# Kernel optimization log

Hardware: AMD Instinct MI355X
Metric: run time of the kernel (lower is better)

Reference implementation:

```python
import jax, jax.numpy as jnp
import numpy as np

D_STATE = 16
D_CONV = 4

def layernorm(x, g, b, eps=1e-5):
    m = jnp.mean(x, -1, keepdims=True)
    v = jnp.var(x, -1, keepdims=True)
    return (x - m) / jnp.sqrt(v + eps) * g + b

def conv1x1(x, w):  # x [b,h,w,cin], w [cin,cout]
    return jnp.einsum('bhwc,cd->bhwd', x, w)

def dwconv3x3(x, w):  # x [b,h,w,C], w [3,3,1,C] (HWIO, groups=C)
    return jax.lax.conv_general_dilated(x, w, (1, 1), 'SAME',
        dimension_numbers=('NHWC', 'HWIO', 'NHWC'),
        feature_group_count=x.shape[-1])

def causal_dwconv1d(x, w, b):  # x [B,L,D], w [K,1,D]; causal depthwise conv (Mamba d_conv=4)
    xp = jnp.pad(x, ((0, 0), (D_CONV - 1, 0), (0, 0)))
    y = jax.lax.conv_general_dilated(xp, w, (1,), 'VALID',
        dimension_numbers=('NWC', 'WIO', 'NWC'),
        feature_group_count=x.shape[-1])
    return y + b

def selective_scan(deltaA, deltaBx, C):
    # deltaA, deltaBx: [B,L,D,S]; C: [B,L,S] -> y: [B,L,D]
    def step(h, inp):
        dA, dBx, c = inp
        h = dA * h + dBx
        return h, jnp.einsum('bds,bs->bd', h, c)
    h0 = jnp.zeros(deltaA.shape[:1] + deltaA.shape[2:], deltaA.dtype)
    _, ys = jax.lax.scan(step, h0,
        (jnp.swapaxes(deltaA, 0, 1), jnp.swapaxes(deltaBx, 0, 1), jnp.swapaxes(C, 0, 1)))
    return jnp.swapaxes(ys, 0, 1)

def spa_ssm(x, in_w, conv_w, conv_b, xproj_w, dt_w, dt_b, Alog, D, out_w):
    # Mamba (slow path) applied to flattened spatial sequence; x: [b,h,w,c]
    b, h, w, c = x.shape
    L = h * w
    xs = x.reshape(b, L, c)
    di = Alog.shape[0]
    xz = xs @ in_w                       # [b,L,2*di]
    xi, z = xz[..., :di], xz[..., di:]
    xi = jax.nn.silu(causal_dwconv1d(xi, conv_w, conv_b))
    dbc = xi @ xproj_w                   # [b,L,dt_rank+2*S]
    dtr = dt_w.shape[0]
    dt = jax.nn.softplus(dbc[..., :dtr] @ dt_w + dt_b)   # [b,L,di]
    B = dbc[..., dtr:dtr + D_STATE]
    C = dbc[..., dtr + D_STATE:]
    A = -jnp.exp(Alog)                   # [di,S]
    deltaA = jnp.exp(dt[..., None] * A)                  # [b,L,di,S]
    deltaBx = (dt * xi)[..., None] * B[:, :, None, :]    # [b,L,di,S]
    y = selective_scan(deltaA, deltaBx, C) + D * xi
    y = y * jax.nn.silu(z)
    return (y @ out_w).reshape(b, h, w, c)

def camba_forward(x, ln1_g, ln1_b, vin_w1, vin_dw, vin_w2, vout_dw1, vout_dw2,
                  ssm_in_w, ssm_conv_w, ssm_conv_b, ssm_xproj_w, ssm_dt_w, ssm_dt_b,
                  ssm_Alog, ssm_D, ssm_out_w, ln2_g, ln2_b, ff_w1, ff_dw, ff_w2):
    x = jnp.transpose(x, (0, 2, 3, 1))   # [b,h,w,c]
    # ESSM: v_in_head = LN -> 1x1 -> dw3x3 -> GELU -> 1x1
    x0 = conv1x1(layernorm(x, ln1_g, ln1_b), vin_w1)
    x0 = jax.nn.gelu(dwconv3x3(x0, vin_dw), approximate=False)
    x0 = conv1x1(x0, vin_w2)
    y = spa_ssm(x0, ssm_in_w, ssm_conv_w, ssm_conv_b, ssm_xproj_w,
                ssm_dt_w, ssm_dt_b, ssm_Alog, ssm_D, ssm_out_w) + x0
    # v_out_head = dw3x3 -> GELU -> dw3x3, residual
    y = dwconv3x3(jax.nn.gelu(dwconv3x3(y, vout_dw1), approximate=False), vout_dw2) + y
    x = y + x                            # block residual
    # PreNorm FeedForward (mult=4): 1x1 -> LReLU -> dw3x3 -> LReLU -> 1x1
    t = layernorm(x, ln2_g, ln2_b)
    t = jax.nn.leaky_relu(conv1x1(t, ff_w1), 0.2)
    t = jax.nn.leaky_relu(dwconv3x3(t, ff_dw), 0.2)
    t = conv1x1(t, ff_w2)
    x = t + x
    return jnp.transpose(x, (0, 3, 1, 2))

def setup_inputs() -> dict:
    key = jax.random.key(0)
    ks = jax.random.split(key, 16)
    b, c, h, w = 8, 64, 64, 64
    di, ds, dtr = 128, 16, 4
    s = 0.05
    n = lambda k, shp: jax.random.normal(k, shp, jnp.float32) * s
    dt0 = jnp.exp(jax.random.uniform(ks[1], (di,)) * (np.log(0.1) - np.log(1e-3)) + np.log(1e-3))
    return dict(
        x=jax.random.normal(ks[0], (b, c, h, w), jnp.float32),
        ln1_g=jnp.ones(c), ln1_b=jnp.zeros(c),
        vin_w1=n(ks[2], (c, c)), vin_dw=n(ks[3], (3, 3, 1, c)), vin_w2=n(ks[4], (c, c)),
        vout_dw1=n(ks[5], (3, 3, 1, c)), vout_dw2=n(ks[6], (3, 3, 1, c)),
        ssm_in_w=n(ks[7], (c, 2 * di)),
        ssm_conv_w=n(ks[8], (D_CONV, 1, di)), ssm_conv_b=jnp.zeros(di),
        ssm_xproj_w=n(ks[9], (di, dtr + 2 * ds)),
        ssm_dt_w=n(ks[10], (dtr, di)), ssm_dt_b=jnp.log(jnp.expm1(dt0)),
        ssm_Alog=jnp.log(jnp.broadcast_to(jnp.arange(1., ds + 1), (di, ds))),
        ssm_D=jnp.ones(di),
        ssm_out_w=n(ks[11], (di, c)),
        ln2_g=jnp.ones(c), ln2_b=jnp.zeros(c),
        ff_w1=n(ks[12], (c, 4 * c)), ff_dw=n(ks[13], (3, 3, 1, 4 * c)), ff_w2=n(ks[14], (4 * c, c)),
    )

def reference(x, ln1_g, ln1_b, vin_w1, vin_dw, vin_w2, vout_dw1, vout_dw2,
              ssm_in_w, ssm_conv_w, ssm_conv_b, ssm_xproj_w, ssm_dt_w, ssm_dt_b,
              ssm_Alog, ssm_D, ssm_out_w, ln2_g, ln2_b, ff_w1, ff_dw, ff_w2):
    return camba_forward(x, ln1_g, ln1_b, vin_w1, vin_dw, vin_w2, vout_dw1, vout_dw2,
                         ssm_in_w, ssm_conv_w, ssm_conv_b, ssm_xproj_w, ssm_dt_w, ssm_dt_b,
                         ssm_Alog, ssm_D, ssm_out_w, ln2_g, ln2_b, ff_w1, ff_dw, ff_w2)
```

## Files before the change

kernel.cpp:

```cpp
#include <hip/hip_runtime.h>
#include <hip/hip_bf16.h>
#include <math.h>

typedef unsigned short u16;
typedef __attribute__((ext_vector_type(8))) short s8v;
typedef __attribute__((ext_vector_type(4))) float f4v;

#define B_    8
#define C_    64
#define HW_   4096
#define NPIX  32768
#define DI    128
#define NCH   256
#define CHL   16

__device__ __forceinline__ float b2f(u16 v){ return __uint_as_float(((unsigned)v)<<16); }
__device__ __forceinline__ u16 f2b(float x){
  unsigned u = __float_as_uint(x);
  u += 0x7fff + ((u >> 16) & 1);
  return (u16)(u >> 16);
}
__device__ __forceinline__ float gelu_exact(float x){ return 0.5f*x*(1.0f+erff(x*0.70710678118654752f)); }
__device__ __forceinline__ float leaky02(float x){ return x>0.f ? x : 0.2f*x; }
__device__ __forceinline__ float softplus_(float x){ return fmaxf(x,0.f)+log1pf(__expf(-fabsf(x))); }
__device__ __forceinline__ float silu_(float x){ return x / (1.0f + __expf(-x)); }
__device__ __forceinline__ void unpack16(uint4 q0, uint4 q1, float* v){
  unsigned w[8]={q0.x,q0.y,q0.z,q0.w,q1.x,q1.y,q1.z,q1.w};
  #pragma unroll
  for(int j=0;j<8;j++){
    v[2*j]   = __uint_as_float(w[j]<<16);
    v[2*j+1] = __uint_as_float(w[j]&0xffff0000u);
  }
}

__global__ void k_prep(const float* __restrict__ vin_w1, const float* __restrict__ vin_w2,
                       const float* __restrict__ ssm_in_w, const float* __restrict__ xproj,
                       const float* __restrict__ dtw, const float* __restrict__ ssm_outw,
                       const float* __restrict__ ff_w1, const float* __restrict__ ff_w2,
                       u16* __restrict__ wv1, u16* __restrict__ wv2, u16* __restrict__ wsi,
                       u16* __restrict__ wdb, u16* __restrict__ wout, u16* __restrict__ wf1,
                       u16* __restrict__ wf2t){
  int g = blockIdx.x*256 + threadIdx.x;
  if(g < 4096){
    int n=g>>6, c=g&63;
    wv1[n*64+c]=f2b(vin_w1[c*64+n]);
    wv2[n*64+c]=f2b(vin_w2[c*64+n]);
  }
  if(g < 16384){
    int n=g>>6, c=g&63;
    wsi[n*64+c]=f2b(ssm_in_w[c*256+n]);
    wf1[n*64+c]=f2b(ff_w1[c*256+n]);
    int n2=g/256, k2=g%256;
    wf2t[n2*256+k2]=f2b(ff_w2[k2*64+n2]);
  }
  if(g < 8192){
    int n=g>>7, k=g&127;
    wout[n*128+k]=f2b(ssm_outw[k*64+n]);
  }
  if(g < 20480){
    int n=g/128, k=g%128;
    float v;
    if(n < 128){
      v = 0.f;
      for(int r=0;r<4;r++) v += xproj[k*36+r]*dtw[r*128+n];
    }else{
      v = xproj[k*36+4+(n-128)];
    }
    wdb[n*128+k]=f2b(v);
  }
}

__global__ __launch_bounds__(256) void k_trans_ln_mm(const float* __restrict__ x,
                     const float* __restrict__ g, const float* __restrict__ bta,
                     const u16* __restrict__ wT,
                     u16* __restrict__ xT, u16* __restrict__ outp){
  const int LDA = 72, NS = 4;
  __shared__ float tile[64][65];
  __shared__ __align__(16) u16 sA[64*LDA];
  __shared__ __align__(16) u16 sW[64*LDA];
  int tid = threadIdx.x;
  int blk = blockIdx.x;
  int b = blk >> 6;
  int hwb = (blk & 63) << 6;
  int lane = tid & 63, row = tid >> 6;
  const float* src = x + (size_t)b*C_*HW_;
  #pragma unroll
  for(int k=0;k<16;k++){
    int c = row + 4*k;
    tile[c][lane] = src[c*HW_ + hwb + lane];
  }
  for(int idx=tid; idx<64*8; idx+=256){
    int n = idx>>3, c8 = (idx&7)*8;
    *(uint4*)(sW + n*LDA + c8) = *(const uint4*)(wT + n*64 + c8);
  }
  __syncthreads();
  u16* dstT = xT + (size_t)b*HW_*C_;
  #pragma unroll
  for(int k=0;k<16;k++){
    int hwl = row + 4*k;
    dstT[(hwb+hwl)*C_ + lane] = f2b(tile[lane][hwl]);
  }
  float gg = g[lane], bb = bta[lane];
  #pragma unroll
  for(int i=0;i<16;i++){
    int hwl = row*16 + i;
    float v = tile[lane][hwl];
    float s = v, sq = v*v;
    #pragma unroll
    for(int o=32;o>0;o>>=1){ s += __shfl_xor(s,o); sq += __shfl_xor(sq,o); }
    float m = s*(1.f/64.f);
    float var = sq*(1.f/64.f) - m*m;
    float r = rsqrtf(var + 1e-5f);
    sA[hwl*LDA + lane] = f2b((v-m)*r*gg + bb);
  }
  __syncthreads();
  int ln = tid & 63, wv = tid >> 6;
  int mrow = ln & 15, quad = ln >> 4;
  f4v acc[NS];
  #pragma unroll
  for(int i=0;i<NS;i++) acc[i] = (f4v){0.f,0.f,0.f,0.f};
  const u16* aBase = sA + (wv*16 + mrow)*LDA + quad*8;
  const u16* wBase = sW + mrow*LDA + quad*8;
  #pragma unroll
  for(int kk=0; kk<64; kk+=32){
    s8v af = *(const s8v*)(aBase + kk);
    #pragma unroll
    for(int ns=0; ns<NS; ns++){
      s8v bf = *(const s8v*)(wBase + ns*16*LDA + kk);
      acc[ns] = __builtin_amdgcn_mfma_f32_16x16x32_bf16(af, bf, acc[ns], 0, 0, 0);
    }
  }
  int p0 = blk*64;
  int pr = p0 + wv*16 + quad*4;
  #pragma unroll
  for(int ns=0; ns<NS; ns++){
    int n = ns*16 + mrow;
    #pragma unroll
    for(int r=0;r<4;r++)
      outp[(size_t)(pr+r)*64 + n] = f2b(acc[ns][r]);
  }
}

__global__ __launch_bounds__(256) void k_dw3mm(const u16* __restrict__ in,
                     const float* __restrict__ dwgt, const u16* __restrict__ wT,
                     u16* __restrict__ x0){
  const int LDT = 72;
  __shared__ __align__(16) u16 sIn[10*10*64];
  __shared__ __align__(16) u16 sT[64*LDT];
  __shared__ __align__(16) u16 sW[64*LDT];
  int tid = threadIdx.x;
  int blk = blockIdx.x;
  int b = blk >> 6;
  int t6 = blk & 63;
  int h0 = (t6 >> 3) * 8, w0 = (t6 & 7) * 8;
  for(int idx=tid; idx<64*8; idx+=256){
    int n = idx>>3, c8 = (idx&7)*8;
    *(uint4*)(sW + n*LDT + c8) = *(const uint4*)(wT + n*64 + c8);
  }
  for(int q=tid; q<10*10*16; q+=256){
    int pp = q >> 4, c4 = q & 15;
    int hh = pp / 10, ww = pp % 10;
    int gh = h0-1+hh, gw = w0-1+ww;
    ushort4 v = make_ushort4(0,0,0,0);
    if((unsigned)gh < 64u && (unsigned)gw < 64u)
      v = *(const ushort4*)(in + (size_t)((b*64+gh)*64+gw)*64 + c4*4);
    *(ushort4*)(sIn + pp*64 + c4*4) = v;
  }
  __syncthreads();
  int c4 = tid & 15;
  #pragma unroll
  for(int pass=0; pass<4; pass++){
    int opix = pass*16 + (tid>>4);
    int oh = opix >> 3, ow = opix & 7;
    float a0=0.f,a1=0.f,a2=0.f,a3=0.f;
    #pragma unroll
    for(int kh=0;kh<3;kh++){
      #pragma unroll
      for(int kw=0;kw<3;kw++){
        ushort4 v = *(const ushort4*)(sIn + ((oh+kh)*10 + (ow+kw))*64 + c4*4);
        float4 wv = *(const float4*)(dwgt + (kh*3+kw)*64 + c4*4);
        a0 += b2f(v.x)*wv.x; a1 += b2f(v.y)*wv.y;
        a2 += b2f(v.z)*wv.z; a3 += b2f(v.w)*wv.w;
      }
    }
    ushort4 o; o.x=f2b(gelu_exact(a0)); o.y=f2b(gelu_exact(a1));
    o.z=f2b(gelu_exact(a2)); o.w=f2b(gelu_exact(a3));
    *(ushort4*)(sT + opix*LDT + c4*4) = o;
  }
  __syncthreads();
  int ln = tid & 63, wv = tid >> 6;
  int mrow = ln & 15, quad = ln >> 4;
  f4v acc[4];
  #pragma unroll
  for(int i=0;i<4;i++) acc[i] = (f4v){0.f,0.f,0.f,0.f};
  const u16* aBase = sT + (wv*16 + mrow)*LDT + quad*8;
  const u16* wBase = sW + mrow*LDT + quad*8;
  #pragma unroll
  for(int kk=0; kk<64; kk+=32){
    s8v af = *(const s8v*)(aBase + kk);
    #pragma unroll
    for(int ns=0; ns<4; ns++){
      s8v bf = *(const s8v*)(wBase + ns*16*LDT + kk);
      acc[ns] = __builtin_amdgcn_mfma_f32_16x16x32_bf16(af, bf, acc[ns], 0, 0, 0);
    }
  }
  #pragma unroll
  for(int ns=0; ns<4; ns++){
    int n = ns*16 + mrow;
    #pragma unroll
    for(int r=0;r<4;r++){
      int opix = wv*16 + quad*4 + r;
      int oh = opix >> 3, ow = opix & 7;
      size_t p = ((size_t)(b*64 + h0+oh)*64 + (w0+ow));
      x0[p*64 + n] = f2b(acc[ns][r]);
    }
  }
}

__global__ __launch_bounds__(256) void k_ssm_dtbc(const u16* __restrict__ wT,
                     const u16* __restrict__ x0,
                     const float* __restrict__ cw, const float* __restrict__ cb,
                     const u16* __restrict__ wdb, const float* __restrict__ dtbias,
                     const float* __restrict__ alog,
                     u16* __restrict__ xi, u16* __restrict__ zs,
                     u16* __restrict__ dtout, u16* __restrict__ bcout,
                     u16* __restrict__ Pb, u16* __restrict__ Qb){
  const int LDA=72, NS=16, LDY=136, LDWD=136, NS2=10, LDD=136;
  __shared__ __align__(16) u16 S[31616];
  u16* sW   = S;
  u16* sA   = S + 18432;
  u16* ubuf = S + 23040;
  u16* xiT  = S;
  u16* wdbS = S + 8704;
  u16* sdt  = S + 8704;
  u16* sbc2 = S + 17408;
  int tid = threadIdx.x;
  int p0 = blockIdx.x*64;
  int ln = tid & 63, wv = tid >> 6;
  int mrow = ln & 15, quad = ln >> 4;
  for(int idx=tid; idx<256*8; idx+=256){
    int n = idx>>3, c8 = (idx&7)*8;
    *(uint4*)(sW + n*LDA + c8) = *(const uint4*)(wT + n*64 + c8);
  }
  for(int g=tid; g<64*8; g+=256){
    int row = g >> 3, c8 = (g & 7)*8;
    *(uint4*)(sA + row*LDA + c8) = *(const uint4*)(x0 + (size_t)(p0+row)*64 + c8);
  }
  __syncthreads();
  f4v acc[NS];
  #pragma unroll
  for(int i=0;i<NS;i++) acc[i] = (f4v){0.f,0.f,0.f,0.f};
  const u16* aBase = sA + (wv*16 + mrow)*LDA + quad*8;
  const u16* wBase = sW + mrow*LDA + quad*8;
  #pragma unroll
  for(int kk=0; kk<64; kk+=32){
    s8v af = *(const s8v*)(aBase + kk);
    #pragma unroll
    for(int ns=0; ns<NS; ns++){
      s8v bf = *(const s8v*)(wBase + ns*16*LDA + kk);
      acc[ns] = __builtin_amdgcn_mfma_f32_16x16x32_bf16(af, bf, acc[ns], 0, 0, 0);
    }
  }
  bool bstart = ((p0 & 4095) == 0);
  for(int idx=tid; idx<384; idx+=256){
    int j = idx >> 7, n = idx & 127;
    float a2 = 0.f;
    if(!bstart){
      const u16* xr = x0 + (size_t)(p0-3+j)*64;
      #pragma unroll 8
      for(int c=0;c<64;c++) a2 += b2f(xr[c]) * b2f(sW[n*LDA+c]);
    }
    ubuf[j*128 + n] = f2b(a2);
  }
  int prl = wv*16 + quad*4;
  #pragma unroll
  for(int ns=0; ns<NS; ns++){
    int n = ns*16 + mrow;
    if(n < 128){
      #pragma unroll
      for(int r=0;r<4;r++) ubuf[(prl+r+3)*128 + n] = f2b(acc[ns][r]);
    }else{
      #pragma unroll
      for(int r=0;r<4;r++) zs[(size_t)(p0+prl+r)*128 + (n-128)] = f2b(silu_(acc[ns][r]));
    }
  }
  __syncthreads();
  int d4 = tid & 31;
  float4 cbv = *(const float4*)(cb + d4*4);
  for(int row = tid >> 5; row < 64; row += 8){
    float a0=cbv.x, a1=cbv.y, a2=cbv.z, a3=cbv.w;
    #pragma unroll
    for(int k=0;k<4;k++){
      ushort4 v = *(const ushort4*)(ubuf + (row+k)*128 + d4*4);
      float4 wv4 = *(const float4*)(cw + k*128 + d4*4);
      a0 += b2f(v.x)*wv4.x; a1 += b2f(v.y)*wv4.y;
      a2 += b2f(v.z)*wv4.z; a3 += b2f(v.w)*wv4.w;
    }
    ushort4 o; o.x=f2b(silu_(a0)); o.y=f2b(silu_(a1)); o.z=f2b(silu_(a2)); o.w=f2b(silu_(a3));
    *(ushort4*)(xi + (size_t)(p0+row)*128 + d4*4) = o;
    *(ushort4*)(xiT + row*LDY + d4*4) = o;
  }
  __syncthreads();
  for(int idx=tid; idx<160*16; idx+=256){
    int n = idx>>4, c8 = (idx&15)*8;
    *(uint4*)(wdbS + n*LDWD + c8) = *(const uint4*)(wdb + n*128 + c8);
  }
  __syncthreads();
  f4v acc2[NS2];
  #pragma unroll
  for(int i=0;i<NS2;i++) acc2[i] = (f4v){0.f,0.f,0.f,0.f};
  #pragma unroll
  for(int kk=0; kk<128; kk+=32){
    s8v af = *(const s8v*)(xiT + (wv*16+mrow)*LDY + kk + quad*8);
    #pragma unroll
    for(int ns=0; ns<NS2; ns++){
      s8v bf = *(const s8v*)(wdbS + (ns*16+mrow)*LDWD + kk + quad*8);
      acc2[ns] = __builtin_amdgcn_mfma_f32_16x16x32_bf16(af, bf, acc2[ns], 0, 0, 0);
    }
  }
  __syncthreads();
  int pr = p0 + prl;
  #pragma unroll
  for(int ns=0; ns<NS2; ns++){
    int n = ns*16 + mrow;
    if(n < 128){
      float bs = dtbias[n];
      #pragma unroll
      for(int r=0;r<4;r++){
        u16 dv = f2b(softplus_(acc2[ns][r] + bs));
        dtout[(size_t)(pr+r)*128 + n] = dv;
        sdt[(prl+r)*LDD + n] = dv;
      }
    }else{
      #pragma unroll
      for(int r=0;r<4;r++){
        u16 bv = f2b(acc2[ns][r]);
        bcout[(size_t)(pr+r)*32 + (n-128)] = bv;
        sbc2[(prl+r)*36 + (n-128)] = bv;
      }
    }
  }
  __syncthreads();
  {
    int d = tid & 127;
    int cp = tid >> 7;
    float A[16];
    #pragma unroll
    for(int s=0;s<16;s++) A[s] = -__expf(alog[d*16+s]);
    int bI = p0 >> 12;
    int chbase = (p0 & 4095) >> 4;
    for(int cc = 2*cp; cc < 2*cp+2; cc++){
      int r0 = cc*16;
      float Q[16], sumdt = 0.f;
      #pragma unroll
      for(int s=0;s<16;s++) Q[s] = 0.f;
      #pragma unroll
      for(int i=0;i<CHL;i++){
        float dtv = b2f(sdt[(r0+i)*LDD + d]);
        float uv  = dtv * b2f(xiT[(r0+i)*LDY + d]);
        sumdt += dtv;
        #pragma unroll
        for(int s=0;s<16;s++){
          float Bv = b2f(sbc2[(r0+i)*36 + s]);
          float a = __expf(dtv*A[s]);
          Q[s] = a*Q[s] + uv*Bv;
        }
      }
      int gidx = (chbase+cc)*16384 + (bI*128+d)*16;
      unsigned pw[8], qw[8];
      #pragma unroll
      for(int j=0;j<8;j++){
        pw[j] = (unsigned)f2b(__expf(A[2*j]*sumdt)) | ((unsigned)f2b(__expf(A[2*j+1]*sumdt))<<16);
        qw[j] = (unsigned)f2b(Q[2*j]) | ((unsigned)f2b(Q[2*j+1])<<16);
      }
      *(uint4*)(Pb+gidx)   = make_uint4(pw[0],pw[1],pw[2],pw[3]);
      *(uint4*)(Pb+gidx+8) = make_uint4(pw[4],pw[5],pw[6],pw[7]);
      *(uint4*)(Qb+gidx)   = make_uint4(qw[0],qw[1],qw[2],qw[3]);
      *(uint4*)(Qb+gidx+8) = make_uint4(qw[4],qw[5],qw[6],qw[7]);
    }
  }
}

__global__ __launch_bounds__(256) void k_scan2(const u16* __restrict__ Pb, const u16* __restrict__ Qb,
                        u16* __restrict__ Hin){
  __shared__ __align__(16) u16 sP[256*32];
  __shared__ __align__(16) u16 sQ[256*32];
  __shared__ float gP[8*32];
  __shared__ float gQ[8*32];
  int tid = threadIdx.x;
  int s0 = blockIdx.x * 32;
  for(int idx = tid; idx < 256*4; idx += 256){
    int ch = idx >> 2, j8 = (idx & 3) * 8;
    *(uint4*)(sP + ch*32 + j8) = *(const uint4*)(Pb + (size_t)ch*16384 + s0 + j8);
    *(uint4*)(sQ + ch*32 + j8) = *(const uint4*)(Qb + (size_t)ch*16384 + s0 + j8);
  }
  __syncthreads();
  int sl = tid & 31, grp = tid >> 5;
  int base = grp * 32;
  float P = 1.f, Q = 0.f;
  #pragma unroll 8
  for(int c = 0; c < 32; c++){
    float p = b2f(sP[(base+c)*32 + sl]);
    float q = b2f(sQ[(base+c)*32 + sl]);
    P = p * P;
    Q = p * Q + q;
  }
  gP[grp*32 + sl] = P;
  gQ[grp*32 + sl] = Q;
  __syncthreads();
  float h = 0.f;
  #pragma unroll
  for(int g = 0; g < 7; g++){
    if(g < grp) h = gP[g*32 + sl] * h + gQ[g*32 + sl];
  }
  for(int c = 0; c < 32; c++){
    Hin[(size_t)(base+c)*16384 + s0 + sl] = f2b(h);
    float p = b2f(sP[(base+c)*32 + sl]);
    float q = b2f(sQ[(base+c)*32 + sl]);
    h = p * h + q;
  }
}

__global__ __launch_bounds__(128) void k_scan3_mm(const u16* __restrict__ dt, const u16* __restrict__ xi,
                        const u16* __restrict__ bc, const u16* __restrict__ zs,
                        const float* __restrict__ alog, const float* __restrict__ Dp,
                        const u16* __restrict__ Hin, const u16* __restrict__ wout,
                        const u16* __restrict__ x0, u16* __restrict__ y){
  const int LDY = 136, LDW = 136;
  int blk = blockIdx.x;
  int ch = blk & (NCH-1);
  int b = blk >> 8;
  int d = threadIdx.x, tid = threadIdx.x;
  __shared__ __align__(16) u16 sY[CHL*LDY];
  __shared__ __align__(16) u16 sWo[64*LDW];
  __shared__ __align__(16) u16 sbc[CHL*32];
  for(int idx=tid; idx<64*16; idx+=128){
    int n = idx>>4, c8 = (idx&15)*8;
    *(uint4*)(sWo + n*LDW + c8) = *(const uint4*)(wout + n*128 + c8);
  }
  int pbase = b*HW_ + ch*CHL;
  if(tid < 64) ((uint4*)sbc)[tid] = ((const uint4*)(bc + (size_t)pbase*32))[tid];
  float A[16], h[16];
  u16 hbuf[16];
  int gidx = ch*16384 + (b*128+d)*16;
  *(uint4*)hbuf     = *(const uint4*)(Hin+gidx);
  *(uint4*)(hbuf+8) = *(const uint4*)(Hin+gidx+8);
  #pragma unroll
  for(int s=0;s<16;s++){ A[s] = -__expf(alog[d*16+s]); h[s] = b2f(hbuf[s]); }
  float Dd = Dp[d];
  float dtv[16], xiv[16], zsv[16];
  #pragma unroll
  for(int i=0;i<CHL;i++){
    dtv[i] = b2f(dt[(size_t)(pbase+i)*128 + d]);
    xiv[i] = b2f(xi[(size_t)(pbase+i)*128 + d]);
    zsv[i] = b2f(zs[(size_t)(pbase+i)*128 + d]);
  }
  __syncthreads();
  #pragma unroll
  for(int i=0;i<CHL;i++){
    float Bv[16], Cv[16];
    unpack16(*(const uint4*)(sbc + i*32),      *(const uint4*)(sbc + i*32 + 8),  Bv);
    unpack16(*(const uint4*)(sbc + i*32 + 16), *(const uint4*)(sbc + i*32 + 24), Cv);
    float u = dtv[i]*xiv[i];
    float acc = Dd*xiv[i];
    #pragma unroll
    for(int s=0;s<16;s++){
      float a = __expf(dtv[i]*A[s]);
      h[s] = a*h[s] + u*Bv[s];
      acc += h[s]*Cv[s];
    }
    sY[i*LDY + d] = f2b(acc * zsv[i]);
  }
  __syncthreads();
  int ln = tid & 63, wv = tid >> 6;
  int mrow = ln & 15, quad = ln >> 4;
  f4v acc2[2];
  acc2[0] = (f4v){0.f,0.f,0.f,0.f};
  acc2[1] = (f4v){0.f,0.f,0.f,0.f};
  #pragma unroll
  for(int kk=0; kk<128; kk+=32){
    s8v af = *(const s8v*)(sY + mrow*LDY + kk + quad*8);
    #pragma unroll
    for(int ns=0; ns<2; ns++){
      int n0 = wv*32 + ns*16;
      s8v bf = *(const s8v*)(sWo + (n0+mrow)*LDW + kk + quad*8);
      acc2[ns] = __builtin_amdgcn_mfma_f32_16x16x32_bf16(af, bf, acc2[ns], 0, 0, 0);
    }
  }
  #pragma unroll
  for(int ns=0; ns<2; ns++){
    int n = wv*32 + ns*16 + mrow;
    #pragma unroll
    for(int r=0;r<4;r++){
      int px = pbase + quad*4 + r;
      y[(size_t)px*64 + n] = f2b(acc2[ns][r] + b2f(x0[(size_t)px*64 + n]));
    }
  }
}

__global__ __launch_bounds__(256) void k_ffn2(const u16* __restrict__ yin,
                     const float* __restrict__ w1, const float* __restrict__ w2,
                     const u16* __restrict__ xTr,
                     const float* __restrict__ g, const float* __restrict__ bta,
                     const u16* __restrict__ wf1, const u16* __restrict__ wf2t,
                     const float* __restrict__ fdw, float* __restrict__ outp){
  const int LDX = 72;
  extern __shared__ __align__(16) u16 S[];
  u16* sX  = S;
  u16* sC  = S + 8064;
  u16* sYh = S + 12672;
  u16* sT  = S + 26784;
  u16* sT1 = S + 12672;
  u16* sW1 = S + 20736;
  u16* sW2 = S + 25344;
  float* sDW = (float*)(S + 29952);
  int tid = threadIdx.x;
  int blk = blockIdx.x;
  int b = blk >> 6;
  int t6 = blk & 63;
  int h0 = (t6 >> 3)*8, w0 = (t6 & 7)*8;
  int ln = tid & 63, wv = tid >> 6;
  int mrow = ln & 15, quad = ln >> 4;
  for(int q=tid; q<196*16; q+=256){
    int pp = q >> 4, c4 = q & 15;
    int hh = pp / 14, ww = pp - hh*14;
    int gh = h0-3+hh, gw = w0-3+ww;
    ushort4 v = make_ushort4(0,0,0,0);
    if((unsigned)gh < 64u && (unsigned)gw < 64u)
      v = *(const ushort4*)(yin + (size_t)((b*64+gh)*64+gw)*64 + c4*4);
    *(ushort4*)(sYh + pp*LDX + c4*4) = v;
  }
  __syncthreads();
  for(int q=tid; q<144*16; q+=256){
    int tpix = q >> 4, c4 = q & 15;
    int th = tpix / 12, tw = tpix - th*12;
    int gh = h0-2+th, gw = w0-2+tw;
    ushort4 o = make_ushort4(0,0,0,0);
    if((unsigned)gh < 64u && (unsigned)gw < 64u){
      float a0=0.f,a1=0.f,a2=0.f,a3=0.f;
      #pragma unroll
      for(int kh=0;kh<3;kh++){
        #pragma unroll
        for(int kw=0;kw<3;kw++){
          ushort4 v = *(const ushort4*)(sYh + ((th+kh)*14 + (tw+kw))*LDX + c4*4);
          float4 wv4 = *(const float4*)(w1 + (kh*3+kw)*64 + c4*4);
          a0 += b2f(v.x)*wv4.x; a1 += b2f(v.y)*wv4.y;
          a2 += b2f(v.z)*wv4.z; a3 += b2f(v.w)*wv4.w;
        }
      }
      o.x=f2b(gelu_exact(a0)); o.y=f2b(gelu_exact(a1));
      o.z=f2b(gelu_exact(a2)); o.w=f2b(gelu_exact(a3));
    }
    *(ushort4*)(sT + tpix*LDX + c4*4) = o;
  }
  __syncthreads();
  for(int q=tid; q<100*16; q+=256){
    int xpix = q >> 4, c4 = q & 15;
    int xh = xpix / 10, xw = xpix - xh*10;
    int gh = h0-1+xh, gw = w0-1+xw;
    ushort4 o = make_ushort4(0,0,0,0);
    if((unsigned)gh < 64u && (unsigned)gw < 64u){
      float a0=0.f,a1=0.f,a2=0.f,a3=0.f;
      #pragma unroll
      for(int kh=0;kh<3;kh++){
        #pragma unroll
        for(int kw=0;kw<3;kw++){
          ushort4 v = *(const ushort4*)(sT + ((xh+kh)*12 + (xw+kw))*LDX + c4*4);
          float4 wv4 = *(const float4*)(w2 + (kh*3+kw)*64 + c4*4);
          a0 += b2f(v.x)*wv4.x; a1 += b2f(v.y)*wv4.y;
          a2 += b2f(v.z)*wv4.z; a3 += b2f(v.w)*wv4.w;
        }
      }
      ushort4 ry = *(const ushort4*)(sYh + ((xh+2)*14 + (xw+2))*LDX + c4*4);
      ushort4 rx = *(const ushort4*)(xTr + (size_t)((b*64+gh)*64+gw)*64 + c4*4);
      a0 += b2f(ry.x) + b2f(rx.x);
      a1 += b2f(ry.y) + b2f(rx.y);
      a2 += b2f(ry.z) + b2f(rx.z);
      a3 += b2f(ry.w) + b2f(rx.w);
      o.x=f2b(a0); o.y=f2b(a1); o.z=f2b(a2); o.w=f2b(a3);
    }
    *(ushort4*)(sX + xpix*LDX + c4*4) = o;
    if(xh>=1 && xh<=8 && xw>=1 && xw<=8)
      *(ushort4*)(sC + ((xh-1)*8 + (xw-1))*LDX + c4*4) = o;
  }
  __syncthreads();
  for(int i=tid; i<9*64; i+=256) ((float4*)sDW)[i] = ((const float4*)fdw)[i];
  float gg = g[ln], bb = bta[ln];
  for(int hp = wv; hp < 112; hp += 4){
    u16 o = 0;
    if(hp < 100){
      int th = hp/10, tw = hp - th*10;
      int gh = h0-1+th, gw = w0-1+tw;
      if((unsigned)gh < 64u && (unsigned)gw < 64u){
        float v = b2f(sX[hp*LDX + ln]);
        float s = v, sq = v*v;
        #pragma unroll
        for(int o2=32;o2>0;o2>>=1){ s += __shfl_xor(s,o2); sq += __shfl_xor(sq,o2); }
        float m = s*(1.f/64.f);
        float var = sq*(1.f/64.f) - m*m;
        float r = rsqrtf(var + 1e-5f);
        o = f2b((v-m)*r*gg + bb);
      }
    }
    sX[hp*LDX + ln] = o;
  }
  f4v acc2[4];
  #pragma unroll
  for(int i=0;i<4;i++) acc2[i] = (f4v){0.f,0.f,0.f,0.f};
  int p = wv*16 + mrow;
  int oh = p >> 3, ow = p & 7;
  for(int c=0; c<4; c++){
    int nc0 = c*64;
    __syncthreads();
    for(int idx=tid; idx<64*8; idx+=256){
      int n = idx>>3, c8 = (idx&7)*8;
      *(uint4*)(sW1 + n*LDX + c8) = *(const uint4*)(wf1 + (size_t)(nc0+n)*64 + c8);
      *(uint4*)(sW2 + n*LDX + c8) = *(const uint4*)(wf2t + (size_t)n*256 + nc0 + c8);
    }
    __syncthreads();
    for(int mt = wv; mt < 7; mt += 4){
      f4v a1[4];
      #pragma unroll
      for(int i=0;i<4;i++) a1[i] = (f4v){0.f,0.f,0.f,0.f};
      const u16* aB = sX + (mt*16 + mrow)*LDX + quad*8;
      const u16* wB = sW1 + mrow*LDX + quad*8;
      #pragma unroll
      for(int kk=0; kk<64; kk+=32){
        s8v af = *(const s8v*)(aB + kk);
        #pragma unroll
        for(int ns=0; ns<4; ns++){
          s8v bf = *(const s8v*)(wB + ns*16*LDX + kk);
          a1[ns] = __builtin_amdgcn_mfma_f32_16x16x32_bf16(af, bf, a1[ns], 0, 0, 0);
        }
      }
      #pragma unroll
      for(int ns=0; ns<4; ns++)
        #pragma unroll
        for(int r=0; r<4; r++)
          sT1[(mt*16 + quad*4 + r)*LDX + ns*16 + mrow] = f2b(leaky02(a1[ns][r]));
    }
    __syncthreads();
    #pragma unroll
    for(int half=0; half<2; half++){
      int ch0 = half*32 + quad*8;
      float a[8];
      #pragma unroll
      for(int j=0;j<8;j++) a[j] = 0.f;
      #pragma unroll
      for(int kh=0;kh<3;kh++){
        #pragma unroll
        for(int kw=0;kw<3;kw++){
          s8v v = *(const s8v*)(sT1 + ((oh+kh)*10 + (ow+kw))*LDX + ch0);
          const float* wp = sDW + (kh*3+kw)*256 + nc0 + ch0;
          float4 w0v = *(const float4*)(wp);
          float4 w1v = *(const float4*)(wp+4);
          a[0] += b2f((u16)v[0])*w0v.x; a[1] += b2f((u16)v[1])*w0v.y;
          a[2] += b2f((u16)v[2])*w0v.z; a[3] += b2f((u16)v[3])*w0v.w;
          a[4] += b2f((u16)v[4])*w1v.x; a[5] += b2f((u16)v[5])*w1v.y;
          a[6] += b2f((u16)v[6])*w1v.z; a[7] += b2f((u16)v[7])*w1v.w;
        }
      }
      s8v af;
      #pragma unroll
      for(int j=0;j<8;j++) af[j] = (short)f2b(leaky02(a[j]));
      #pragma unroll
      for(int ns=0; ns<4; ns++){
        s8v bf = *(const s8v*)(sW2 + (ns*16 + mrow)*LDX + half*32 + quad*8);
        acc2[ns] = __builtin_amdgcn_mfma_f32_16x16x32_bf16(af, bf, acc2[ns], 0, 0, 0);
      }
    }
  }
  int pe = wv*16 + quad*4;
  int eoh = pe >> 3, eow0 = pe & 7;
  #pragma unroll
  for(int ns=0; ns<4; ns++){
    int n = ns*16 + mrow;
    float4 v4;
    v4.x = acc2[ns][0] + b2f(sC[(pe+0)*LDX + n]);
    v4.y = acc2[ns][1] + b2f(sC[(pe+1)*LDX + n]);
    v4.z = acc2[ns][2] + b2f(sC[(pe+2)*LDX + n]);
    v4.w = acc2[ns][3] + b2f(sC[(pe+3)*LDX + n]);
    *(float4*)(outp + (size_t)b*C_*HW_ + (size_t)n*HW_ + (h0+eoh)*64 + (w0+eow0)) = v4;
  }
}

extern "C" void kernel_launch(void* const* d_in, const int* in_sizes, int n_in,
                              void* d_out, int out_size, void* d_ws, size_t ws_size,
                              hipStream_t stream) {
  const float* x        = (const float*)d_in[0];
  const float* ln1_g    = (const float*)d_in[1];
  const float* ln1_b    = (const float*)d_in[2];
  const float* vin_w1   = (const float*)d_in[3];
  const float* vin_dw   = (const float*)d_in[4];
  const float* vin_w2   = (const float*)d_in[5];
  const float* vout_dw1 = (const float*)d_in[6];
  const float* vout_dw2 = (const float*)d_in[7];
  const float* ssm_in_w = (const float*)d_in[8];
  const float* ssm_cw   = (const float*)d_in[9];
  const float* ssm_cb   = (const float*)d_in[10];
  const float* ssm_xprj = (const float*)d_in[11];
  const float* ssm_dtw  = (const float*)d_in[12];
  const float* ssm_dtb  = (const float*)d_in[13];
  const float* ssm_Alog = (const float*)d_in[14];
  const float* ssm_D    = (const float*)d_in[15];
  const float* ssm_outw = (const float*)d_in[16];
  const float* ln2_g    = (const float*)d_in[17];
  const float* ln2_b    = (const float*)d_in[18];
  const float* ff_w1    = (const float*)d_in[19];
  const float* ff_dw    = (const float*)d_in[20];
  const float* ff_w2    = (const float*)d_in[21];
  float* out = (float*)d_out;

  const size_t M = 1u<<20;
  u16* U   = (u16*)d_ws;
  u16* xT  = U;
  u16* tA  = U + 2*M;
  u16* tB  = U + 4*M;
  u16* x0  = U + 6*M;
  u16* xi  = U + 8*M;
  u16* zs  = U + 12*M;
  u16* dtb = U + 24*M;
  u16* bc  = U + 28*M;
  u16* Pb  = U + 16*M;
  u16* Qb  = U + 20*M;
  u16* Hin = tA;
  u16* y   = U + 16*M;
  u16* wv1  = U + 33*M;
  u16* wv2  = wv1 + 4096;
  u16* wsi  = wv2 + 4096;
  u16* wdb  = wsi + 16384;
  u16* wout = wdb + 20480;
  u16* wf1  = wout + 8192;
  u16* wf2t = wf1 + 16384;

  static bool attr_set = false;
  if(!attr_set){
    hipFuncSetAttribute((const void*)k_ffn2,
                        hipFuncAttributeMaxDynamicSharedMemorySize, 74304);
    attr_set = true;
  }

  k_prep<<<80,256,0,stream>>>(vin_w1, vin_w2, ssm_in_w, ssm_xprj, ssm_dtw, ssm_outw,
                              ff_w1, ff_w2, wv1, wv2, wsi, wdb, wout, wf1, wf2t);

  k_trans_ln_mm<<<512,256,0,stream>>>(x, ln1_g, ln1_b, wv1, xT, tB);
  k_dw3mm<<<512,256,0,stream>>>(tB, vin_dw, wv2, x0);

  k_ssm_dtbc<<<512,256,0,stream>>>(wsi, x0, ssm_cw, ssm_cb, wdb, ssm_dtb, ssm_Alog,
                                   xi, zs, dtb, bc, Pb, Qb);
  k_scan2<<<512,256,0,stream>>>(Pb, Qb, Hin);
  k_scan3_mm<<<2048,128,0,stream>>>(dtb, xi, bc, zs, ssm_Alog, ssm_D, Hin, wout, x0, y);

  k_ffn2<<<512,256,74304,stream>>>(y, vout_dw1, vout_dw2, xT, ln2_g, ln2_b,
                                   wf1, wf2t, ff_dw, out);
}
```

Measured before the change: 258.3 us.

## Split chunk-local scan out of dt/BC GEMM kernel into separate kernel

Moves the per-chunk selective-scan pass (computing chunk decay P and partial state Q) out of k_ssm_dtbc into a new k_scan1 kernel. The new kernel gives one thread per (batch, chunk, channel) across 1024 blocks and reads dt, xi and B/C back from global memory. Before, only 256 threads per block ran that pass after a barrier. The aim is more parallelism for the exp-heavy scan and lighter register and shared-memory pressure in the GEMM kernel. The cost is an extra launch and a re-read of dt, xi and bc from global memory.

```diff
diff --git a/kernel.cpp b/kernel.cpp
--- a/kernel.cpp
+++ b/kernel.cpp
@@ -221,19 +221,15 @@
                      const u16* __restrict__ x0,
                      const float* __restrict__ cw, const float* __restrict__ cb,
                      const u16* __restrict__ wdb, const float* __restrict__ dtbias,
-                     const float* __restrict__ alog,
                      u16* __restrict__ xi, u16* __restrict__ zs,
-                     u16* __restrict__ dtout, u16* __restrict__ bcout,
-                     u16* __restrict__ Pb, u16* __restrict__ Qb){
-  const int LDA=72, NS=16, LDY=136, LDWD=136, NS2=10, LDD=136;
+                     u16* __restrict__ dtout, u16* __restrict__ bcout){
+  const int LDA=72, NS=16, LDY=136, LDWD=136, NS2=10;
   __shared__ __align__(16) u16 S[31616];
   u16* sW   = S;
   u16* sA   = S + 18432;
   u16* ubuf = S + 23040;
   u16* xiT  = S;
   u16* wdbS = S + 8704;
-  u16* sdt  = S + 8704;
-  u16* sbc2 = S + 17408;
   int tid = threadIdx.x;
   int p0 = blockIdx.x*64;
   int ln = tid & 63, wv = tid >> 6;
@@ -318,67 +314,66 @@
       acc2[ns] = __builtin_amdgcn_mfma_f32_16x16x32_bf16(af, bf, acc2[ns], 0, 0, 0);
     }
   }
-  __syncthreads();
-  int pr = p0 + prl;
+  int pr = p0 + wv*16 + quad*4;
   #pragma unroll
   for(int ns=0; ns<NS2; ns++){
     int n = ns*16 + mrow;
     if(n < 128){
       float bs = dtbias[n];
       #pragma unroll
-      for(int r=0;r<4;r++){
-        u16 dv = f2b(softplus_(acc2[ns][r] + bs));
-        dtout[(size_t)(pr+r)*128 + n] = dv;
-        sdt[(prl+r)*LDD + n] = dv;
-      }
+      for(int r=0;r<4;r++)
+        dtout[(size_t)(pr+r)*128 + n] = f2b(softplus_(acc2[ns][r] + bs));
     }else{
       #pragma unroll
-      for(int r=0;r<4;r++){
-        u16 bv = f2b(acc2[ns][r]);
-        bcout[(size_t)(pr+r)*32 + (n-128)] = bv;
-        sbc2[(prl+r)*36 + (n-128)] = bv;
-      }
-    }
-  }
-  __syncthreads();
-  {
-    int d = tid & 127;
-    int cp = tid >> 7;
-    float A[16];
-    #pragma unroll
-    for(int s=0;s<16;s++) A[s] = -__expf(alog[d*16+s]);
-    int bI = p0 >> 12;
-    int chbase = (p0 & 4095) >> 4;
-    for(int cc = 2*cp; cc < 2*cp+2; cc++){
-      int r0 = cc*16;
-      float Q[16], sumdt = 0.f;
-      #pragma unroll
-      for(int s=0;s<16;s++) Q[s] = 0.f;
-      #pragma unroll
-      for(int i=0;i<CHL;i++){
-        float dtv = b2f(sdt[(r0+i)*LDD + d]);
-        float uv  = dtv * b2f(xiT[(r0+i)*LDY + d]);
-        sumdt += dtv;
-        #pragma unroll
-        for(int s=0;s<16;s++){
-          float Bv = b2f(sbc2[(r0+i)*36 + s]);
-          float a = __expf(dtv*A[s]);
-          Q[s] = a*Q[s] + uv*Bv;
-        }
-      }
-      int gidx = (chbase+cc)*16384 + (bI*128+d)*16;
-      unsigned pw[8], qw[8];
-      #pragma unroll
-      for(int j=0;j<8;j++){
-        pw[j] = (unsigned)f2b(__expf(A[2*j]*sumdt)) | ((unsigned)f2b(__expf(A[2*j+1]*sumdt))<<16);
-        qw[j] = (unsigned)f2b(Q[2*j]) | ((unsigned)f2b(Q[2*j+1])<<16);
-      }
-      *(uint4*)(Pb+gidx)   = make_uint4(pw[0],pw[1],pw[2],pw[3]);
-      *(uint4*)(Pb+gidx+8) = make_uint4(pw[4],pw[5],pw[6],pw[7]);
-      *(uint4*)(Qb+gidx)   = make_uint4(qw[0],qw[1],qw[2],qw[3]);
-      *(uint4*)(Qb+gidx+8) = make_uint4(qw[4],qw[5],qw[6],qw[7]);
-    }
-  }
+      for(int r=0;r<4;r++)
+        bcout[(size_t)(pr+r)*32 + (n-128)] = f2b(acc2[ns][r]);
+    }
+  }
+}
+
+__global__ __launch_bounds__(256) void k_scan1(const u16* __restrict__ dt, const u16* __restrict__ xi,
+                        const u16* __restrict__ bc, const float* __restrict__ alog,
+                        u16* __restrict__ Pb, u16* __restrict__ Qb){
+  int t = blockIdx.x*256 + threadIdx.x;
+  int d = t & 127;
+  int ch = (t >> 7) & 255;
+  int b = t >> 15;
+  int pbase = b*HW_ + ch*CHL;
+  float A[16];
+  #pragma unroll
+  for(int s=0;s<16;s++) A[s] = -__expf(alog[d*16+s]);
+  float dtv[16], uv[16];
+  #pragma unroll
+  for(int i=0;i<CHL;i++){
+    dtv[i] = b2f(dt[(size_t)(pbase+i)*128 + d]);
+    uv[i]  = dtv[i] * b2f(xi[(size_t)(pbase+i)*128 + d]);
+  }
+  float Q[16], sumdt = 0.f;
+  #pragma unroll
+  for(int s=0;s<16;s++) Q[s] = 0.f;
+  #pragma unroll
+  for(int i=0;i<CHL;i++){
+    float Bv[16];
+    unpack16(*(const uint4*)(bc + (size_t)(pbase+i)*32),
+             *(const uint4*)(bc + (size_t)(pbase+i)*32 + 8), Bv);
+    sumdt += dtv[i];
+    #pragma unroll
+    for(int s=0;s<16;s++){
+      float a = __expf(dtv[i]*A[s]);
+      Q[s] = a*Q[s] + uv[i]*Bv[s];
+    }
+  }
+  int gidx = ch*16384 + (b*128+d)*16;
+  unsigned pw[8], qw[8];
+  #pragma unroll
+  for(int j=0;j<8;j++){
+    pw[j] = (unsigned)f2b(__expf(A[2*j]*sumdt)) | ((unsigned)f2b(__expf(A[2*j+1]*sumdt))<<16);
+    qw[j] = (unsigned)f2b(Q[2*j]) | ((unsigned)f2b(Q[2*j+1])<<16);
+  }
+  *(uint4*)(Pb+gidx)   = make_uint4(pw[0],pw[1],pw[2],pw[3]);
+  *(uint4*)(Pb+gidx+8) = make_uint4(pw[4],pw[5],pw[6],pw[7]);
+  *(uint4*)(Qb+gidx)   = make_uint4(qw[0],qw[1],qw[2],qw[3]);
+  *(uint4*)(Qb+gidx+8) = make_uint4(qw[4],qw[5],qw[6],qw[7]);
 }
 
 __global__ __launch_bounds__(256) void k_scan2(const u16* __restrict__ Pb, const u16* __restrict__ Qb,
@@ -746,8 +741,9 @@
   k_trans_ln_mm<<<512,256,0,stream>>>(x, ln1_g, ln1_b, wv1, xT, tB);
   k_dw3mm<<<512,256,0,stream>>>(tB, vin_dw, wv2, x0);
 
-  k_ssm_dtbc<<<512,256,0,stream>>>(wsi, x0, ssm_cw, ssm_cb, wdb, ssm_dtb, ssm_Alog,
-                                   xi, zs, dtb, bc, Pb, Qb);
+  k_ssm_dtbc<<<512,256,0,stream>>>(wsi, x0, ssm_cw, ssm_cb, wdb, ssm_dtb,
+                                   xi, zs, dtb, bc);
+  k_scan1<<<1024,256,0,stream>>>(dtb, xi, bc, ssm_Alog, Pb, Qb);
   k_scan2<<<512,256,0,stream>>>(Pb, Qb, Hin);
   k_scan3_mm<<<2048,128,0,stream>>>(dtb, xi, bc, zs, ssm_Alog, ssm_D, Hin, wout, x0, y);
 
```

Result: faster. 246.0 us (median of 3 runs) (-4.7%).
